# Performance work log

Measured on AMD Instinct MI355X. Metric: run time of the kernel, lower is better.

Reference implementation:

```python
import jax, jax.numpy as jnp
import numpy as np

B, S_ENC, S_DEC, D_ENC, D_DEC, UNITS = 8, 256, 128, 512, 512, 512


def setup_inputs() -> dict:
    key = jax.random.key(0)
    ks = jax.random.split(key, 5)
    enc_scale = 1.0 / np.sqrt(D_ENC)
    dec_scale = 1.0 / np.sqrt(D_DEC)
    u_scale = 1.0 / np.sqrt(UNITS)
    return {
        "encodings": jax.random.normal(ks[0], (B, S_ENC, D_ENC), dtype=jnp.float32),
        "decodings": jax.random.normal(ks[1], (B, S_DEC, D_DEC), dtype=jnp.float32),
        "W_enc": jax.random.normal(ks[2], (D_ENC, UNITS), dtype=jnp.float32) * enc_scale,
        "W_dec": jax.random.normal(ks[3], (D_DEC, UNITS), dtype=jnp.float32) * dec_scale,
        "W_score": jax.random.normal(ks[4], (UNITS, 1), dtype=jnp.float32) * u_scale,
        "bias_enc": jnp.zeros((UNITS,), dtype=jnp.float32),
        "bias_dec": jnp.zeros((UNITS,), dtype=jnp.float32),
        "bias_score": jnp.zeros((1,), dtype=jnp.float32),
    }


def reference(encodings, decodings, W_enc, W_dec, W_score, bias_enc, bias_dec, bias_score):
    # activation='linear' -> identity after the bias add
    d_enc = jnp.einsum("bed,du->beu", encodings, W_enc) + bias_enc  # [B, S_enc, U]
    d_dec = jnp.einsum("bqd,du->bqu", decodings, W_dec) + bias_dec  # [B, S_dec, U]
    # Bahdanau additive scores: tanh(dec_proj + enc_proj) broadcast to [B, S_dec, S_enc, U]
    tanh_add = jnp.tanh(d_dec[:, :, None, :] + d_enc[:, None, :, :])
    scores = jnp.einsum("bqeu,u->bqe", tanh_add, W_score[:, 0]) + bias_score[0]
    weights = jax.nn.softmax(scores, axis=-1)  # softmax over encoder positions
    # weighted sum of raw encodings -> [B, S_dec, D_enc]
    contexts = jnp.einsum("bqe,bed->bqd", weights, encodings)
    return contexts
```

## Files before the change

### kernel.cpp

```cpp
#include <hip/hip_runtime.h>
#include <hip/hip_fp16.h>

typedef __attribute__((ext_vector_type(8))) _Float16 f16x8;
typedef __attribute__((ext_vector_type(4))) float f32x4;
typedef __attribute__((ext_vector_type(2))) __fp16 fp16x2;

__device__ inline unsigned int pack_f16(float x, float y) {
    union { fp16x2 h; unsigned int u; } c;
    c.h = __builtin_amdgcn_cvt_pkrtz(x, y);
    return c.u;
}
__device__ inline float2 unpack_f16(unsigned int u) {
    union { unsigned int u32; __half2 h2; } c; c.u32 = u;
    return __half22float2(c.h2);
}

__global__ __launch_bounds__(256) void prep_w(
    const float* __restrict__ Wenc, const float* __restrict__ Wdec,
    const float* __restrict__ enc,  const float* __restrict__ dec,
    unsigned short* __restrict__ WeT, unsigned short* __restrict__ WdT,
    unsigned short* __restrict__ enc16, unsigned short* __restrict__ dec16)
{
    __shared__ float L[64][65];
    const int bid = blockIdx.x;
    const int t = threadIdx.x;
    if (bid >= 128) {
        const float* src; unsigned int* dst;
        if (bid < 192) { int blk = bid - 128; src = enc + (size_t)blk * 16384;
                         dst = (unsigned int*)enc16 + (size_t)blk * 8192; }
        else           { int blk = bid - 192; src = dec + (size_t)blk * 16384;
                         dst = (unsigned int*)dec16 + (size_t)blk * 8192; }
#pragma unroll 4
        for (int i = 0; i < 16; ++i) {
            int off = (i << 10) + (t << 2);
            float4 v = *(const float4*)(src + off);
            *(uint2*)(dst + (off >> 1)) =
                make_uint2(pack_f16(v.x, v.y), pack_f16(v.z, v.w));
        }
        return;
    }
    const float* W = (bid < 64) ? Wenc : Wdec;
    unsigned short* T = (bid < 64) ? WeT : WdT;
    const int tb = bid & 63;
    const int d0 = (tb >> 3) << 6, u0v = (tb & 7) << 6;
    {
        const int c4 = (t & 15) << 2;
#pragma unroll
        for (int i = 0; i < 4; ++i) {
            int row = (i << 4) + (t >> 4);
            float4 v = *(const float4*)&W[(size_t)(d0 + row) * 512 + u0v + c4];
            L[row][c4 + 0] = v.x;
            L[row][c4 + 1] = v.y;
            L[row][c4 + 2] = v.z;
            L[row][c4 + 3] = v.w;
        }
    }
    __syncthreads();
    const int u = t >> 2, dg = t & 3;
    unsigned int hw[8];
#pragma unroll
    for (int j = 0; j < 8; ++j) {
        float x0 = L[(dg << 4) + (j << 1) + 0][u];
        float x1 = L[(dg << 4) + (j << 1) + 1][u];
        hw[j] = pack_f16(x0, x1);
    }
    size_t ob = (size_t)(u0v + u) * 512 + d0 + (dg << 4);
    *(uint4*)&T[ob]     = make_uint4(hw[0], hw[1], hw[2], hw[3]);
    *(uint4*)&T[ob + 8] = make_uint4(hw[4], hw[5], hw[6], hw[7]);
}

__global__ __launch_bounds__(128, 1) void proj_kernel(
    const unsigned short* __restrict__ enc16, const unsigned short* __restrict__ dec16,
    const unsigned short* __restrict__ WeT,   const unsigned short* __restrict__ WdT,
    const float* __restrict__ bias_enc, const float* __restrict__ bias_dec,
    unsigned short* __restrict__ EH,
    float* __restrict__ Gq4)
{
    const float Cs = 2.8853900817779268f;
    const int bid = blockIdx.x;
    const int t = threadIdx.x;
    const int lane = t & 63, wr = t >> 6;
    const int frow = lane & 15, quad = lane >> 4;
    const int ko = quad << 3;

    const unsigned short *pa0, *pa1, *pb0, *pb1;
    if (bid < 512) {
        const int b = bid & 7, s = bid >> 3;
        const int u0 = ((s & 7) << 6) + (wr << 5);
        const int e0 = (s >> 3) << 5;
        pa0 = WeT + (size_t)(u0 + frow) * 512 + ko;
        pa1 = pa0 + 16 * 512;
        pb0 = enc16 + (size_t)((b << 8) + e0 + frow) * 512 + ko;
        pb1 = pb0 + 16 * 512;
    } else {
        const int s = bid - 512;
        const int b = s & 7, s2 = s >> 3;
        const int q0 = ((s2 >> 4) << 6) + (wr << 5);
        const int u0 = (s2 & 15) << 5;
        pa0 = dec16 + (size_t)((b << 7) + q0 + frow) * 512 + ko;
        pa1 = pa0 + 16 * 512;
        pb0 = WdT + (size_t)(u0 + frow) * 512 + ko;
        pb1 = pb0 + 16 * 512;
    }

    f16x8 sa0[4], sa1[4], sb0[4], sb1[4];
    auto LD = [&](int st, int k) {
        sa0[st] = *(const f16x8*)(pa0 + k);
        sa1[st] = *(const f16x8*)(pa1 + k);
        sb0[st] = *(const f16x8*)(pb0 + k);
        sb1[st] = *(const f16x8*)(pb1 + k);
    };
    f32x4 acc[2][2] = {{{0.f,0.f,0.f,0.f},{0.f,0.f,0.f,0.f}},
                       {{0.f,0.f,0.f,0.f},{0.f,0.f,0.f,0.f}}};
    LD(0, 0); LD(1, 32); LD(2, 64); LD(3, 96);
    for (int k0 = 0; k0 < 512; k0 += 128) {
#pragma unroll
        for (int st = 0; st < 4; ++st) {
            acc[0][0] = __builtin_amdgcn_mfma_f32_16x16x32_f16(sa0[st], sb0[st], acc[0][0], 0, 0, 0);
            acc[0][1] = __builtin_amdgcn_mfma_f32_16x16x32_f16(sa0[st], sb1[st], acc[0][1], 0, 0, 0);
            acc[1][0] = __builtin_amdgcn_mfma_f32_16x16x32_f16(sa1[st], sb0[st], acc[1][0], 0, 0, 0);
            acc[1][1] = __builtin_amdgcn_mfma_f32_16x16x32_f16(sa1[st], sb1[st], acc[1][1], 0, 0, 0);
            LD(st, (k0 + 128 + (st << 5)) & 511);
        }
    }

    if (bid < 512) {
        const int b = bid & 7, s = bid >> 3;
        const int u0 = ((s & 7) << 6) + (wr << 5);
        const int e0 = (s >> 3) << 5;
#pragma unroll
        for (int fm = 0; fm < 2; ++fm)
#pragma unroll
            for (int fn = 0; fn < 2; ++fn) {
                int ub = u0 + (fm << 4) + (quad << 2);
                int e  = e0 + (fn << 4) + frow;
                float4 bi = *(const float4*)&bias_enc[ub];
                float E0 = __builtin_amdgcn_exp2f((acc[fm][fn][0] + bi.x) * Cs);
                float E1 = __builtin_amdgcn_exp2f((acc[fm][fn][1] + bi.y) * Cs);
                float E2 = __builtin_amdgcn_exp2f((acc[fm][fn][2] + bi.z) * Cs);
                float E3 = __builtin_amdgcn_exp2f((acc[fm][fn][3] + bi.w) * Cs);
                ((uint2*)EH)[(((size_t)(b << 7) + (ub >> 2)) << 8) + e] =
                    make_uint2(pack_f16(E0, E1), pack_f16(E2, E3));
            }
    } else {
        const int s = bid - 512;
        const int b = s & 7, s2 = s >> 3;
        const int q0 = ((s2 >> 4) << 6) + (wr << 5);
        const int u0 = (s2 & 15) << 5;
#pragma unroll
        for (int fm = 0; fm < 2; ++fm)
#pragma unroll
            for (int fn = 0; fn < 2; ++fn) {
                int qb = q0 + (fm << 4) + (quad << 2);
                int u  = u0 + (fn << 4) + frow;
                float bi = bias_dec[u];
                size_t base = (((size_t)(b << 5) + (qb >> 2)) << 11) + (u << 2);
#pragma unroll
                for (int g = 0; g < 4; ++g)
                    Gq4[base + g] =
                        __builtin_amdgcn_exp2f((acc[fm][fn][g] + bi) * Cs);
            }
    }
}

__global__ __launch_bounds__(1024, 4) void attend_kernel(
    const unsigned short* __restrict__ enc16,
    const unsigned short* __restrict__ EH,
    const float* __restrict__ Gq4,
    const float* __restrict__ Wscore,
    float* __restrict__ out)
{
    __shared__ float smem[8192];
    __shared__ float wT[256][4];

    const float LOG2E = 1.4426950408889634f;

    const int bid = blockIdx.x;
    const int b = bid & 7;
    const int qt = (bid >> 3) & 31;
    const int q0 = qt << 2;
    const int tid = threadIdx.x;
    const int wv = tid >> 6, lane = tid & 63;

    const int e  = ((wv & 3) << 6) + lane;
    const int uq = wv >> 2;
    const int u0 = __builtin_amdgcn_readfirstlane(uq << 7);

    const uint2* Ep = (const uint2*)EH + (((size_t)(b << 7) + (u0 >> 2)) << 8) + e;
    const float* Gq = Gq4 + (((size_t)(b << 5) + qt) << 11);
    const float* Wp = Wscore + u0;

    float a0 = 0.f, a1 = 0.f, a2 = 0.f, a3 = 0.f;
    uint2 de = Ep[0];
    float4 g0 = *(const float4*)(Gq + ((u0 + 0) << 2));
    float4 g1 = *(const float4*)(Gq + ((u0 + 1) << 2));
    float4 g2 = *(const float4*)(Gq + ((u0 + 2) << 2));
    float4 g3 = *(const float4*)(Gq + ((u0 + 3) << 2));
    float4 w4 = *(const float4*)(Wp);
    for (int g = 0; g < 32; ++g) {
        uint2 cde = de;
        float4 cg0 = g0, cg1 = g1, cg2 = g2, cg3 = g3, cw = w4;
        if (g < 31) {
            int un = u0 + ((g + 1) << 2);
            de = Ep[(size_t)(g + 1) << 8];
            g0 = *(const float4*)(Gq + ((un + 0) << 2));
            g1 = *(const float4*)(Gq + ((un + 1) << 2));
            g2 = *(const float4*)(Gq + ((un + 2) << 2));
            g3 = *(const float4*)(Gq + ((un + 3) << 2));
            w4 = *(const float4*)(Wp + (g + 1 - g/32) * 0 + ((g + 1) << 2));
        }
        float2 f01 = unpack_f16(cde.x);
        float2 f23 = unpack_f16(cde.y);
        float E;
        E = f01.x;
        a0 = fmaf(cw.x, __builtin_amdgcn_rcpf(fmaf(E, cg0.x, 1.f)), a0);
        a1 = fmaf(cw.x, __builtin_amdgcn_rcpf(fmaf(E, cg0.y, 1.f)), a1);
        a2 = fmaf(cw.x, __builtin_amdgcn_rcpf(fmaf(E, cg0.z, 1.f)), a2);
        a3 = fmaf(cw.x, __builtin_amdgcn_rcpf(fmaf(E, cg0.w, 1.f)), a3);
        E = f01.y;
        a0 = fmaf(cw.y, __builtin_amdgcn_rcpf(fmaf(E, cg1.x, 1.f)), a0);
        a1 = fmaf(cw.y, __builtin_amdgcn_rcpf(fmaf(E, cg1.y, 1.f)), a1);
        a2 = fmaf(cw.y, __builtin_amdgcn_rcpf(fmaf(E, cg1.z, 1.f)), a2);
        a3 = fmaf(cw.y, __builtin_amdgcn_rcpf(fmaf(E, cg1.w, 1.f)), a3);
        E = f23.x;
        a0 = fmaf(cw.z, __builtin_amdgcn_rcpf(fmaf(E, cg2.x, 1.f)), a0);
        a1 = fmaf(cw.z, __builtin_amdgcn_rcpf(fmaf(E, cg2.y, 1.f)), a1);
        a2 = fmaf(cw.z, __builtin_amdgcn_rcpf(fmaf(E, cg2.z, 1.f)), a2);
        a3 = fmaf(cw.z, __builtin_amdgcn_rcpf(fmaf(E, cg2.w, 1.f)), a3);
        E = f23.y;
        a0 = fmaf(cw.w, __builtin_amdgcn_rcpf(fmaf(E, cg3.x, 1.f)), a0);
        a1 = fmaf(cw.w, __builtin_amdgcn_rcpf(fmaf(E, cg3.y, 1.f)), a1);
        a2 = fmaf(cw.w, __builtin_amdgcn_rcpf(fmaf(E, cg3.z, 1.f)), a2);
        a3 = fmaf(cw.w, __builtin_amdgcn_rcpf(fmaf(E, cg3.w, 1.f)), a3);
    }
    smem[((uq << 2) + 0) * 256 + e] = a0;
    smem[((uq << 2) + 1) * 256 + e] = a1;
    smem[((uq << 2) + 2) * 256 + e] = a2;
    smem[((uq << 2) + 3) * 256 + e] = a3;
    __syncthreads();

    if (wv < 4) {
        const int q = wv;
        float l[4];
        float m = -1e30f;
#pragma unroll
        for (int i = 0; i < 4; ++i) {
            int ee = lane + (i << 6);
            float a = smem[(0 + q) * 256 + ee] + smem[(4 + q) * 256 + ee] +
                      smem[(8 + q) * 256 + ee] + smem[(12 + q) * 256 + ee];
            l[i] = -2.f * a;
            m = fmaxf(m, l[i]);
        }
#pragma unroll
        for (int mk = 32; mk >= 1; mk >>= 1) m = fmaxf(m, __shfl_xor(m, mk, 64));
        float p[4];
        float ssum = 0.f;
#pragma unroll
        for (int i = 0; i < 4; ++i) {
            p[i] = __builtin_amdgcn_exp2f((l[i] - m) * LOG2E);
            ssum += p[i];
        }
#pragma unroll
        for (int mk = 32; mk >= 1; mk >>= 1) ssum += __shfl_xor(ssum, mk, 64);
        float inv = __builtin_amdgcn_rcpf(ssum);
#pragma unroll
        for (int i = 0; i < 4; ++i) wT[lane + (i << 6)][q] = p[i] * inv;
    }
    __syncthreads();

    {
        const int dp = tid & 255;
        float p0x = 0.f, p0y = 0.f, p1x = 0.f, p1y = 0.f;
        float p2x = 0.f, p2y = 0.f, p3x = 0.f, p3y = 0.f;
        const unsigned int* ep = (const unsigned int*)enc16 +
                                 (((size_t)(b << 8) + (uq << 6)) << 8) + dp;
#pragma unroll 4
        for (int ee = 0; ee < 64; ++ee) {
            float2 x = unpack_f16(ep[(size_t)ee << 8]);
            float4 w = *(const float4*)&wT[(uq << 6) + ee][0];
            p0x = fmaf(w.x, x.x, p0x); p0y = fmaf(w.x, x.y, p0y);
            p1x = fmaf(w.y, x.x, p1x); p1y = fmaf(w.y, x.y, p1y);
            p2x = fmaf(w.z, x.x, p2x); p2y = fmaf(w.z, x.y, p2y);
            p3x = fmaf(w.w, x.x, p3x); p3y = fmaf(w.w, x.y, p3y);
        }
        float2* sc = (float2*)smem;
        sc[((uq << 2) + 0) * 256 + dp] = make_float2(p0x, p0y);
        sc[((uq << 2) + 1) * 256 + dp] = make_float2(p1x, p1y);
        sc[((uq << 2) + 2) * 256 + dp] = make_float2(p2x, p2y);
        sc[((uq << 2) + 3) * 256 + dp] = make_float2(p3x, p3y);
        __syncthreads();
        const int q = tid >> 8;
        float2 s0 = sc[(0 + q) * 256 + dp];
        float2 s1 = sc[(4 + q) * 256 + dp];
        float2 s2 = sc[(8 + q) * 256 + dp];
        float2 s3 = sc[(12 + q) * 256 + dp];
        float2 o = make_float2(s0.x + s1.x + s2.x + s3.x,
                               s0.y + s1.y + s2.y + s3.y);
        *(float2*)&out[(size_t)((b << 7) + q0 + q) * 512 + (dp << 1)] = o;
    }
}

extern "C" void kernel_launch(void* const* d_in, const int* in_sizes, int n_in,
                              void* d_out, int out_size, void* d_ws, size_t ws_size,
                              hipStream_t stream) {
    const float* enc      = (const float*)d_in[0];
    const float* dec      = (const float*)d_in[1];
    const float* Wenc     = (const float*)d_in[2];
    const float* Wdec     = (const float*)d_in[3];
    const float* Wscore   = (const float*)d_in[4];
    const float* bias_enc = (const float*)d_in[5];
    const float* bias_dec = (const float*)d_in[6];
    float* out = (float*)d_out;

    float* ws = (float*)d_ws;
    unsigned short* EH  = (unsigned short*)ws;
    float* Gq4          = ws + 524288;
    unsigned short* WeT = (unsigned short*)(ws + 1048576);
    unsigned short* WdT = WeT + 262144;
    unsigned short* enc16 = WdT + 262144;
    unsigned short* dec16 = enc16 + 1048576;

    prep_w<<<224, 256, 0, stream>>>(Wenc, Wdec, enc, dec, WeT, WdT, enc16, dec16);
    proj_kernel<<<768, 128, 0, stream>>>(enc16, dec16, WeT, WdT,
                                         bias_enc, bias_dec, EH, Gq4);
    attend_kernel<<<256, 1024, 0, stream>>>(enc16, EH, Gq4, Wscore, out);
}
```

Measured before the change: 110.5 us.

## Combine four reciprocal terms into one division and use packed f32x2 math

The score loop summed w_i/(1+E*g_i) over four units, using one reciprocal per term. It now merges the four fractions into a single numerator over a product denominator, so one rcp covers four units. The arithmetic is written as two-wide float vectors so the compiler can emit packed FMA/mul instructions on CDNA. The weighted-sum loop is also vectorised to f32x2. The cost is extra multiplies and a risk of overflow or precision loss when the four-way product denominator grows large.

```diff
diff --git a/kernel.cpp b/kernel.cpp
--- a/kernel.cpp
+++ b/kernel.cpp
@@ -3,6 +3,7 @@
 
 typedef __attribute__((ext_vector_type(8))) _Float16 f16x8;
 typedef __attribute__((ext_vector_type(4))) float f32x4;
+typedef __attribute__((ext_vector_type(2))) float f32x2;
 typedef __attribute__((ext_vector_type(2))) __fp16 fp16x2;
 
 __device__ inline unsigned int pack_f16(float x, float y) {
@@ -190,7 +191,7 @@
     const float* Gq = Gq4 + (((size_t)(b << 5) + qt) << 11);
     const float* Wp = Wscore + u0;
 
-    float a0 = 0.f, a1 = 0.f, a2 = 0.f, a3 = 0.f;
+    f32x2 accLo = {0.f, 0.f}, accHi = {0.f, 0.f};
     uint2 de = Ep[0];
     float4 g0 = *(const float4*)(Gq + ((u0 + 0) << 2));
     float4 g1 = *(const float4*)(Gq + ((u0 + 1) << 2));
@@ -207,36 +208,48 @@
             g1 = *(const float4*)(Gq + ((un + 1) << 2));
             g2 = *(const float4*)(Gq + ((un + 2) << 2));
             g3 = *(const float4*)(Gq + ((un + 3) << 2));
-            w4 = *(const float4*)(Wp + (g + 1 - g/32) * 0 + ((g + 1) << 2));
+            w4 = *(const float4*)(Wp + ((g + 1) << 2));
         }
         float2 f01 = unpack_f16(cde.x);
         float2 f23 = unpack_f16(cde.y);
-        float E;
-        E = f01.x;
-        a0 = fmaf(cw.x, __builtin_amdgcn_rcpf(fmaf(E, cg0.x, 1.f)), a0);
-        a1 = fmaf(cw.x, __builtin_amdgcn_rcpf(fmaf(E, cg0.y, 1.f)), a1);
-        a2 = fmaf(cw.x, __builtin_amdgcn_rcpf(fmaf(E, cg0.z, 1.f)), a2);
-        a3 = fmaf(cw.x, __builtin_amdgcn_rcpf(fmaf(E, cg0.w, 1.f)), a3);
-        E = f01.y;
-        a0 = fmaf(cw.y, __builtin_amdgcn_rcpf(fmaf(E, cg1.x, 1.f)), a0);
-        a1 = fmaf(cw.y, __builtin_amdgcn_rcpf(fmaf(E, cg1.y, 1.f)), a1);
-        a2 = fmaf(cw.y, __builtin_amdgcn_rcpf(fmaf(E, cg1.z, 1.f)), a2);
-        a3 = fmaf(cw.y, __builtin_amdgcn_rcpf(fmaf(E, cg1.w, 1.f)), a3);
-        E = f23.x;
-        a0 = fmaf(cw.z, __builtin_amdgcn_rcpf(fmaf(E, cg2.x, 1.f)), a0);
-        a1 = fmaf(cw.z, __builtin_amdgcn_rcpf(fmaf(E, cg2.y, 1.f)), a1);
-        a2 = fmaf(cw.z, __builtin_amdgcn_rcpf(fmaf(E, cg2.z, 1.f)), a2);
-        a3 = fmaf(cw.z, __builtin_amdgcn_rcpf(fmaf(E, cg2.w, 1.f)), a3);
-        E = f23.y;
-        a0 = fmaf(cw.w, __builtin_amdgcn_rcpf(fmaf(E, cg3.x, 1.f)), a0);
-        a1 = fmaf(cw.w, __builtin_amdgcn_rcpf(fmaf(E, cg3.y, 1.f)), a1);
-        a2 = fmaf(cw.w, __builtin_amdgcn_rcpf(fmaf(E, cg3.z, 1.f)), a2);
-        a3 = fmaf(cw.w, __builtin_amdgcn_rcpf(fmaf(E, cg3.w, 1.f)), a3);
-    }
-    smem[((uq << 2) + 0) * 256 + e] = a0;
-    smem[((uq << 2) + 1) * 256 + e] = a1;
-    smem[((uq << 2) + 2) * 256 + e] = a2;
-    smem[((uq << 2) + 3) * 256 + e] = a3;
+        const float E0 = f01.x, E1 = f01.y, E2 = f23.x, E3 = f23.y;
+        {
+            f32x2 gl0 = {cg0.x, cg0.y}, gl1 = {cg1.x, cg1.y};
+            f32x2 gl2 = {cg2.x, cg2.y}, gl3 = {cg3.x, cg3.y};
+            f32x2 X = E0 * gl0 + 1.0f;
+            f32x2 Y = E1 * gl1 + 1.0f;
+            f32x2 Z = E2 * gl2 + 1.0f;
+            f32x2 V = E3 * gl3 + 1.0f;
+            f32x2 pxy = X * Y, pzw = Z * V;
+            f32x2 den = pxy * pzw;
+            f32x2 nxy = cw.x * Y + cw.y * X;
+            f32x2 nzw = cw.z * V + cw.w * Z;
+            f32x2 num = nxy * pzw + nzw * pxy;
+            f32x2 r = { __builtin_amdgcn_rcpf(den.x),
+                        __builtin_amdgcn_rcpf(den.y) };
+            accLo += num * r;
+        }
+        {
+            f32x2 gh0 = {cg0.z, cg0.w}, gh1 = {cg1.z, cg1.w};
+            f32x2 gh2 = {cg2.z, cg2.w}, gh3 = {cg3.z, cg3.w};
+            f32x2 X = E0 * gh0 + 1.0f;
+            f32x2 Y = E1 * gh1 + 1.0f;
+            f32x2 Z = E2 * gh2 + 1.0f;
+            f32x2 V = E3 * gh3 + 1.0f;
+            f32x2 pxy = X * Y, pzw = Z * V;
+            f32x2 den = pxy * pzw;
+            f32x2 nxy = cw.x * Y + cw.y * X;
+            f32x2 nzw = cw.z * V + cw.w * Z;
+            f32x2 num = nxy * pzw + nzw * pxy;
+            f32x2 r = { __builtin_amdgcn_rcpf(den.x),
+                        __builtin_amdgcn_rcpf(den.y) };
+            accHi += num * r;
+        }
+    }
+    smem[((uq << 2) + 0) * 256 + e] = accLo.x;
+    smem[((uq << 2) + 1) * 256 + e] = accLo.y;
+    smem[((uq << 2) + 2) * 256 + e] = accHi.x;
+    smem[((uq << 2) + 3) * 256 + e] = accHi.y;
     __syncthreads();
 
     if (wv < 4) {
@@ -270,24 +283,25 @@
 
     {
         const int dp = tid & 255;
-        float p0x = 0.f, p0y = 0.f, p1x = 0.f, p1y = 0.f;
-        float p2x = 0.f, p2y = 0.f, p3x = 0.f, p3y = 0.f;
+        f32x2 p0 = {0.f, 0.f}, p1 = {0.f, 0.f};
+        f32x2 p2 = {0.f, 0.f}, p3 = {0.f, 0.f};
         const unsigned int* ep = (const unsigned int*)enc16 +
                                  (((size_t)(b << 8) + (uq << 6)) << 8) + dp;
 #pragma unroll 4
         for (int ee = 0; ee < 64; ++ee) {
-            float2 x = unpack_f16(ep[(size_t)ee << 8]);
+            float2 xf = unpack_f16(ep[(size_t)ee << 8]);
+            f32x2 x = {xf.x, xf.y};
             float4 w = *(const float4*)&wT[(uq << 6) + ee][0];
-            p0x = fmaf(w.x, x.x, p0x); p0y = fmaf(w.x, x.y, p0y);
-            p1x = fmaf(w.y, x.x, p1x); p1y = fmaf(w.y, x.y, p1y);
-            p2x = fmaf(w.z, x.x, p2x); p2y = fmaf(w.z, x.y, p2y);
-            p3x = fmaf(w.w, x.x, p3x); p3y = fmaf(w.w, x.y, p3y);
+            p0 += w.x * x;
+            p1 += w.y * x;
+            p2 += w.z * x;
+            p3 += w.w * x;
         }
         float2* sc = (float2*)smem;
-        sc[((uq << 2) + 0) * 256 + dp] = make_float2(p0x, p0y);
-        sc[((uq << 2) + 1) * 256 + dp] = make_float2(p1x, p1y);
-        sc[((uq << 2) + 2) * 256 + dp] = make_float2(p2x, p2y);
-        sc[((uq << 2) + 3) * 256 + dp] = make_float2(p3x, p3y);
+        sc[((uq << 2) + 0) * 256 + dp] = make_float2(p0.x, p0.y);
+        sc[((uq << 2) + 1) * 256 + dp] = make_float2(p1.x, p1.y);
+        sc[((uq << 2) + 2) * 256 + dp] = make_float2(p2.x, p2.y);
+        sc[((uq << 2) + 3) * 256 + dp] = make_float2(p3.x, p3.y);
         __syncthreads();
         const int q = tid >> 8;
         float2 s0 = sc[(0 + q) * 256 + dp];
```

Result: faster. 107.4 us (-2.8%).
